# Kernel optimization log

Measured on AMD Instinct MI355X. Metric: run time of the kernel, lower is better.

The kernel has to match this reference:

```python
import jax, jax.numpy as jnp
import numpy as np

N = 8192      # number of nodes; input feature dim == N (identity-style features)
HID = 200     # hidden dim hard-coded in GCNConv(adj.shape[0], 200)
OUT = 5       # out_dim (sentiment classes)


def setup_inputs() -> dict:
    key = jax.random.key(0)
    k1, k2, k3, k4 = jax.random.split(key, 4)
    x = jax.random.normal(k1, (N, N), dtype=jnp.float32)
    adj = jax.random.uniform(k2, (N, N), dtype=jnp.float32)
    W1 = jax.random.normal(k3, (N, HID), dtype=jnp.float32) * (1.0 / np.sqrt(N))
    b1 = jnp.zeros((HID,), dtype=jnp.float32)
    W2 = jax.random.normal(k4, (HID, OUT), dtype=jnp.float32) * (1.0 / np.sqrt(HID))
    b2 = jnp.zeros((OUT,), dtype=jnp.float32)
    return {"x": x, "adj": adj, "W1": W1, "b1": b1, "W2": W2, "b2": b2}


def gcn_conv(adj, x, W, b):
    # support = X @ W (cheap, small output dim), then propagate: adj @ support
    return adj @ (x @ W) + b


def reference(x, adj, W1, b1, W2, b2):
    h = jax.nn.relu(gcn_conv(adj, x, W1, b1))      # [N, 200]
    logits = gcn_conv(adj, h, W2, b2)              # [N, 5]
    return jax.nn.softmax(logits, axis=-1)
```

## Files before the change

kernel.cpp:

```cpp
#include <hip/hip_runtime.h>
#include <hip/hip_fp16.h>
#include <math.h>

#define NN   8192
#define KD   8192
#define HID  200
#define NP   224
#define OUTC 5

#define BM   128
#define BK   32
#define KS   8
#define KCH  (KD / KS)
#define NT   (KCH / BK)
#define LPAD 40

typedef _Float16 f16;
typedef __attribute__((ext_vector_type(4))) _Float16 f16x4;
typedef __attribute__((ext_vector_type(8))) _Float16 f16x8;
typedef __attribute__((ext_vector_type(4))) float f32x4;

__global__ __launch_bounds__(256) void k_prep_w1(const float* __restrict__ W1,
                                                 f16* __restrict__ BfT) {
    __shared__ float tile[64][65];
    const int k0 = blockIdx.x * 64;
    const int n0 = blockIdx.y * 64;
    const int t = threadIdx.x;
    #pragma unroll
    for (int p = 0; p < 16; ++p) {
        int idx = t + p * 256;
        int kk = idx >> 6, nn = idx & 63;
        int n = n0 + nn;
        float v = (n < HID) ? W1[(size_t)(k0 + kk) * HID + n] : 0.0f;
        tile[kk][nn] = v;
    }
    __syncthreads();
    #pragma unroll
    for (int p = 0; p < 16; ++p) {
        int idx = t + p * 256;
        int nn = idx >> 6, kk = idx & 63;
        int n = n0 + nn;
        if (n < NP) BfT[(size_t)n * KD + k0 + kk] = (f16)tile[kk][nn];
    }
}

__global__ __launch_bounds__(512, 4) void k_gemm(const float* __restrict__ A,
                                                 const f16* __restrict__ BfT,
                                                 f16* __restrict__ CP) {
    __shared__ __align__(16) f16 Ah[BM * LPAD];
    __shared__ __align__(16) f16 Al[BM * LPAD];
    __shared__ __align__(16) f16 Bf[NP * LPAD];

    const int t = threadIdx.x;
    const int lane = t & 63;
    const int wave = t >> 6;
    const int wm = wave >> 1, wn = wave & 1;
    const int l15 = lane & 15, g = lane >> 4;
    const int m0 = blockIdx.x * BM;
    const size_t kc0 = (size_t)blockIdx.y * KCH;

    const int arow = t >> 2, aq = t & 3;
    const int br0 = t >> 2, bq0 = t & 3;
    const int u1 = t + 512;
    const int br1 = u1 >> 2, bq1 = u1 & 3;
    const bool hasB1 = (t < 384);

    const float* Aptr = A + (size_t)(m0 + arow) * KD + kc0 + (size_t)aq * 8;
    const f16* B0p = BfT + (size_t)br0 * KD + kc0 + (size_t)bq0 * 8;
    const f16* B1p = BfT + (size_t)br1 * KD + kc0 + (size_t)bq1 * 8;

    f32x4 acc[2][7];
    #pragma unroll
    for (int m = 0; m < 2; ++m)
        #pragma unroll
        for (int n = 0; n < 7; ++n) acc[m][n] = (f32x4){0.f, 0.f, 0.f, 0.f};

    float4 v0, v1;
    f16x8 gb0, gb1;

    auto LOAD = [&](int ks) {
        v0 = *(const float4*)(Aptr + ks);
        v1 = *(const float4*)(Aptr + ks + 4);
        gb0 = *(const f16x8*)(B0p + ks);
        if (hasB1) gb1 = *(const f16x8*)(B1p + ks);
    };
    auto STORE = [&]() {
        f16x8 hv, lv;
        float vv[8] = {v0.x, v0.y, v0.z, v0.w, v1.x, v1.y, v1.z, v1.w};
        #pragma unroll
        for (int j = 0; j < 8; ++j) {
            f16 h = (f16)vv[j];
            hv[j] = h;
            lv[j] = (f16)(vv[j] - (float)h);
        }
        *(f16x8*)&Ah[arow * LPAD + aq * 8] = hv;
        *(f16x8*)&Al[arow * LPAD + aq * 8] = lv;
        *(f16x8*)&Bf[br0 * LPAD + bq0 * 8] = gb0;
        if (hasB1) *(f16x8*)&Bf[br1 * LPAD + bq1 * 8] = gb1;
    };

    LOAD(0);
    for (int i = 0; i < NT; ++i) {
        __syncthreads();
        STORE();
        __syncthreads();
        if (i + 1 < NT) LOAD((i + 1) * BK);

        f16x8 a_h[2], a_l[2];
        #pragma unroll
        for (int m = 0; m < 2; ++m) {
            int r = wm * 32 + m * 16 + l15;
            a_h[m] = *(const f16x8*)&Ah[r * LPAD + g * 8];
            a_l[m] = *(const f16x8*)&Al[r * LPAD + g * 8];
        }
        __builtin_amdgcn_s_setprio(1);
        #pragma unroll
        for (int n = 0; n < 7; ++n) {
            int c = wn * 112 + n * 16 + l15;
            f16x8 b = *(const f16x8*)&Bf[c * LPAD + g * 8];
            #pragma unroll
            for (int m = 0; m < 2; ++m) {
                acc[m][n] = __builtin_amdgcn_mfma_f32_16x16x32_f16(a_l[m], b, acc[m][n], 0, 0, 0);
                acc[m][n] = __builtin_amdgcn_mfma_f32_16x16x32_f16(a_h[m], b, acc[m][n], 0, 0, 0);
            }
        }
        __builtin_amdgcn_s_setprio(0);
    }

    f16* o = CP + (size_t)blockIdx.y * ((size_t)NN * NP);
    #pragma unroll
    for (int m = 0; m < 2; ++m) {
        #pragma unroll
        for (int n = 0; n < 7; ++n) {
            int rb = m0 + wm * 32 + m * 16 + g * 4;
            int c = wn * 112 + n * 16 + l15;
            #pragma unroll
            for (int r = 0; r < 4; ++r)
                o[(size_t)(rb + r) * NP + c] = (f16)acc[m][n][r];
        }
    }
}

__global__ __launch_bounds__(256) void k_combine_split(const f16* __restrict__ CP,
                                                       f16* __restrict__ SfT) {
    __shared__ float tile[64][65];
    const size_t SZ = (size_t)NN * NP;
    const int m0 = blockIdx.x * 64;
    const int n0 = blockIdx.y * 64;
    const int t = threadIdx.x;
    #pragma unroll
    for (int gq = 0; gq < 4; ++gq) {
        int idx4 = t + gq * 256;
        int mm = idx4 >> 4;
        int nn4 = (idx4 & 15) * 4;
        int n = n0 + nn4;
        float s0 = 0.f, s1 = 0.f, s2 = 0.f, s3 = 0.f;
        if (n + 4 <= NP) {
            #pragma unroll
            for (int p = 0; p < KS; ++p) {
                f16x4 v = *(const f16x4*)(CP + (size_t)p * SZ + (size_t)(m0 + mm) * NP + n);
                s0 += (float)v[0]; s1 += (float)v[1]; s2 += (float)v[2]; s3 += (float)v[3];
            }
        }
        tile[mm][nn4 + 0] = s0; tile[mm][nn4 + 1] = s1;
        tile[mm][nn4 + 2] = s2; tile[mm][nn4 + 3] = s3;
    }
    __syncthreads();
    #pragma unroll
    for (int p = 0; p < 16; ++p) {
        int idx = t + p * 256;
        int nn = idx >> 6, mm = idx & 63;
        int n = n0 + nn;
        if (n < NP) SfT[(size_t)n * KD + m0 + mm] = (f16)tile[mm][nn];
    }
}

__global__ __launch_bounds__(256) void k_combine_bias_relu(const f16* __restrict__ CP,
                                                           const float* __restrict__ b1,
                                                           float* __restrict__ H) {
    const size_t SZ = (size_t)NN * NP;
    const int row = blockIdx.x;
    const int t = threadIdx.x;
    if (t < NP) {
        size_t off = (size_t)row * NP + t;
        float s = 0.f;
        #pragma unroll
        for (int p = 0; p < KS; ++p) s += (float)CP[off + p * SZ];
        s += (t < HID) ? b1[t] : 0.0f;
        H[off] = fmaxf(s, 0.0f);
    }
}

__global__ __launch_bounds__(256) void k_hw2(const float* __restrict__ H,
                                             const float* __restrict__ W2,
                                             float* __restrict__ S2T) {
    const int t = threadIdx.x;
    const int wave = t >> 6, lane = t & 63;
    const int row = blockIdx.x * 4 + wave;
    float acc[OUTC] = {0.f, 0.f, 0.f, 0.f, 0.f};
    for (int j = lane; j < HID; j += 64) {
        float h = H[(size_t)row * NP + j];
        #pragma unroll
        for (int c = 0; c < OUTC; ++c) acc[c] += h * W2[j * OUTC + c];
    }
    #pragma unroll
    for (int c = 0; c < OUTC; ++c)
        #pragma unroll
        for (int off = 32; off; off >>= 1) acc[c] += __shfl_down(acc[c], off, 64);
    if (lane == 0) {
        #pragma unroll
        for (int c = 0; c < OUTC; ++c) S2T[(size_t)c * NN + row] = acc[c];
    }
}

__global__ __launch_bounds__(256) void k_final(const float* __restrict__ adj,
                                               const float* __restrict__ S2T,
                                               const float* __restrict__ b2,
                                               float* __restrict__ out) {
    __shared__ float red[4][8][OUTC];
    const int t = threadIdx.x, wave = t >> 6, lane = t & 63;
    const int row0 = blockIdx.x * 8;
    float acc[8][OUTC];
    #pragma unroll
    for (int r = 0; r < 8; ++r)
        #pragma unroll
        for (int c = 0; c < OUTC; ++c) acc[r][c] = 0.f;

    for (int jj = 0; jj < 8; ++jj) {
        int kb = (t + jj * 256) * 4;
        float4 s2[OUTC];
        #pragma unroll
        for (int c = 0; c < OUTC; ++c) s2[c] = *(const float4*)(S2T + (size_t)c * NN + kb);
        #pragma unroll
        for (int r = 0; r < 8; ++r) {
            float4 a = *(const float4*)(adj + (size_t)(row0 + r) * KD + kb);
            #pragma unroll
            for (int c = 0; c < OUTC; ++c)
                acc[r][c] += a.x * s2[c].x + a.y * s2[c].y + a.z * s2[c].z + a.w * s2[c].w;
        }
    }
    #pragma unroll
    for (int r = 0; r < 8; ++r)
        #pragma unroll
        for (int c = 0; c < OUTC; ++c) {
            float v = acc[r][c];
            #pragma unroll
            for (int off = 32; off; off >>= 1) v += __shfl_down(v, off, 64);
            if (lane == 0) red[wave][r][c] = v;
        }
    __syncthreads();
    if (t < 8) {
        int r = t;
        float lg[OUTC];
        #pragma unroll
        for (int c = 0; c < OUTC; ++c)
            lg[c] = red[0][r][c] + red[1][r][c] + red[2][r][c] + red[3][r][c] + b2[c];
        float mx = lg[0];
        #pragma unroll
        for (int c = 1; c < OUTC; ++c) mx = fmaxf(mx, lg[c]);
        float e[OUTC], s = 0.f;
        #pragma unroll
        for (int c = 0; c < OUTC; ++c) { e[c] = expf(lg[c] - mx); s += e[c]; }
        float inv = 1.0f / s;
        #pragma unroll
        for (int c = 0; c < OUTC; ++c) out[(size_t)(row0 + r) * OUTC + c] = e[c] * inv;
    }
}

extern "C" void kernel_launch(void* const* d_in, const int* in_sizes, int n_in,
                              void* d_out, int out_size, void* d_ws, size_t ws_size,
                              hipStream_t stream) {
    const float* x   = (const float*)d_in[0];
    const float* adj = (const float*)d_in[1];
    const float* W1  = (const float*)d_in[2];
    const float* b1  = (const float*)d_in[3];
    const float* W2  = (const float*)d_in[4];
    const float* b2  = (const float*)d_in[5];
    float* out = (float*)d_out;

    char* ws = (char*)d_ws;
    const size_t SPLIT_BYTES = (size_t)NP * KD * sizeof(f16);
    f16*   W1fT = (f16*)(ws);
    f16*   S1fT = (f16*)(ws + SPLIT_BYTES);
    float* H    = (float*)(ws + 2 * SPLIT_BYTES);
    float* S2T  = (float*)(ws + 2 * SPLIT_BYTES + (size_t)NN * NP * sizeof(float));
    f16*   CPf  = (f16*)(ws + 2 * SPLIT_BYTES + (size_t)NN * NP * sizeof(float)
                            + (size_t)OUTC * NN * sizeof(float));

    k_prep_w1<<<dim3(KD / 64, (NP + 63) / 64), 256, 0, stream>>>(W1, W1fT);
    k_gemm<<<dim3(NN / BM, KS), 512, 0, stream>>>(x, W1fT, CPf);
    k_combine_split<<<dim3(NN / 64, (NP + 63) / 64), 256, 0, stream>>>(CPf, S1fT);
    k_gemm<<<dim3(NN / BM, KS), 512, 0, stream>>>(adj, S1fT, CPf);
    k_combine_bias_relu<<<NN, 256, 0, stream>>>(CPf, b1, H);
    k_hw2<<<NN / 4, 256, 0, stream>>>(H, W2, S2T);
    k_final<<<NN / 8, 256, 0, stream>>>(adj, S2T, b2, out);
}
```

Measured before the change: 267.5 us.

## Drop hi/lo fp16 split, use direct global-to-LDS loads with swizzled B layout

The GEMM kernel stops splitting A into high and low fp16 halves, which halves the MFMA count but lowers the precision of the fp32 inputs. It doubles BK to 64 and pre-swizzles B into a tile-contiguous layout so B can be copied straight into LDS with global_load_lds. Manual waitcnt and barrier scheduling replace the two __syncthreads per iteration. The combine and hw2 kernels are vectorised and H is stored in fp16, with some accuracy risk against the fp32 reference.

```diff
diff --git a/kernel.cpp b/kernel.cpp
--- a/kernel.cpp
+++ b/kernel.cpp
@@ -9,65 +9,78 @@
 #define OUTC 5
 
 #define BM   128
-#define BK   32
+#define BK   64
 #define KS   8
 #define KCH  (KD / KS)
 #define NT   (KCH / BK)
-#define LPAD 40
+#define TUB  1792
 
 typedef _Float16 f16;
 typedef __attribute__((ext_vector_type(4))) _Float16 f16x4;
 typedef __attribute__((ext_vector_type(8))) _Float16 f16x8;
 typedef __attribute__((ext_vector_type(4))) float f32x4;
 
+__device__ __forceinline__ void fill16(const f16* g, f16* l) {
+    __builtin_amdgcn_global_load_lds(
+        (const __attribute__((address_space(1))) void*)g,
+        (__attribute__((address_space(3))) void*)l, 16, 0, 0);
+}
+
 __global__ __launch_bounds__(256) void k_prep_w1(const float* __restrict__ W1,
-                                                 f16* __restrict__ BfT) {
+                                                 f16* __restrict__ Bsw) {
     __shared__ float tile[64][65];
-    const int k0 = blockIdx.x * 64;
+    const int kt = blockIdx.x;
     const int n0 = blockIdx.y * 64;
+    const int k0 = kt * 64;
     const int t = threadIdx.x;
     #pragma unroll
-    for (int p = 0; p < 16; ++p) {
-        int idx = t + p * 256;
-        int kk = idx >> 6, nn = idx & 63;
-        int n = n0 + nn;
-        float v = (n < HID) ? W1[(size_t)(k0 + kk) * HID + n] : 0.0f;
-        tile[kk][nn] = v;
+    for (int q = 0; q < 4; ++q) {
+        int idx4 = t + q * 256;
+        int kk = idx4 >> 4, nn4 = (idx4 & 15) * 4;
+        int n = n0 + nn4;
+        float4 v = {0.f, 0.f, 0.f, 0.f};
+        if (n + 4 <= HID) v = *(const float4*)(W1 + (size_t)(k0 + kk) * HID + n);
+        tile[kk][nn4 + 0] = v.x; tile[kk][nn4 + 1] = v.y;
+        tile[kk][nn4 + 2] = v.z; tile[kk][nn4 + 3] = v.w;
     }
     __syncthreads();
     #pragma unroll
-    for (int p = 0; p < 16; ++p) {
-        int idx = t + p * 256;
-        int nn = idx >> 6, kk = idx & 63;
-        int n = n0 + nn;
-        if (n < NP) BfT[(size_t)n * KD + k0 + kk] = (f16)tile[kk][nn];
+    for (int p2 = 0; p2 < 2; ++p2) {
+        int u = t + p2 * 256;
+        int rl = u >> 3, cphys = u & 7;
+        int r = n0 + rl;
+        if (r < NP) {
+            int ck = cphys ^ (r & 7);
+            f16x8 o;
+            #pragma unroll
+            for (int h = 0; h < 8; ++h) o[h] = (f16)tile[ck * 8 + h][rl];
+            *(f16x8*)(Bsw + ((size_t)kt * TUB + r * 8 + cphys) * 8) = o;
+        }
     }
 }
 
 __global__ __launch_bounds__(512, 4) void k_gemm(const float* __restrict__ A,
-                                                 const f16* __restrict__ BfT,
+                                                 const f16* __restrict__ Bsw,
                                                  f16* __restrict__ CP) {
-    __shared__ __align__(16) f16 Ah[BM * LPAD];
-    __shared__ __align__(16) f16 Al[BM * LPAD];
-    __shared__ __align__(16) f16 Bf[NP * LPAD];
+    __shared__ __align__(16) f16 Ah[BM * BK];
+    __shared__ __align__(16) f16 Bf[NP * BK];
 
     const int t = threadIdx.x;
-    const int lane = t & 63;
-    const int wave = t >> 6;
-    const int wm = wave >> 1, wn = wave & 1;
+    const int lane = t & 63, wv = t >> 6;
+    const int wm = wv >> 1, wn = wv & 1;
     const int l15 = lane & 15, g = lane >> 4;
     const int m0 = blockIdx.x * BM;
+    const int kt0 = blockIdx.y * NT;
     const size_t kc0 = (size_t)blockIdx.y * KCH;
 
-    const int arow = t >> 2, aq = t & 3;
-    const int br0 = t >> 2, bq0 = t & 3;
-    const int u1 = t + 512;
-    const int br1 = u1 >> 2, bq1 = u1 & 3;
-    const bool hasB1 = (t < 384);
-
-    const float* Aptr = A + (size_t)(m0 + arow) * KD + kc0 + (size_t)aq * 8;
-    const f16* B0p = BfT + (size_t)br0 * KD + kc0 + (size_t)bq0 * 8;
-    const f16* B1p = BfT + (size_t)br1 * KD + kc0 + (size_t)bq1 * 8;
+    const int ar = t >> 2;
+    const int ac = (t & 3) * 2;
+    const int swzA = ar & 7;
+    f16* aw0 = &Ah[(ar * 8 + ((ac + 0) ^ swzA)) * 8];
+    f16* aw1 = &Ah[(ar * 8 + ((ac + 1) ^ swzA)) * 8];
+    const float* ap = A + (size_t)(m0 + ar) * KD + kc0 + (size_t)(t & 3) * 16;
+
+    const f16* bsrc = Bsw + ((size_t)kt0 * TUB + (size_t)(wv * 64 + lane)) * 8;
 
     f32x4 acc[2][7];
     #pragma unroll
@@ -75,57 +88,61 @@
         #pragma unroll
         for (int n = 0; n < 7; ++n) acc[m][n] = (f32x4){0.f, 0.f, 0.f, 0.f};
 
-    float4 v0, v1;
-    f16x8 gb0, gb1;
-
-    auto LOAD = [&](int ks) {
-        v0 = *(const float4*)(Aptr + ks);
-        v1 = *(const float4*)(Aptr + ks + 4);
-        gb0 = *(const f16x8*)(B0p + ks);
-        if (hasB1) gb1 = *(const f16x8*)(B1p + ks);
-    };
-    auto STORE = [&]() {
-        f16x8 hv, lv;
-        float vv[8] = {v0.x, v0.y, v0.z, v0.w, v1.x, v1.y, v1.z, v1.w};
-        #pragma unroll
-        for (int j = 0; j < 8; ++j) {
-            f16 h = (f16)vv[j];
-            hv[j] = h;
-            lv[j] = (f16)(vv[j] - (float)h);
-        }
-        *(f16x8*)&Ah[arow * LPAD + aq * 8] = hv;
-        *(f16x8*)&Al[arow * LPAD + aq * 8] = lv;
-        *(f16x8*)&Bf[br0 * LPAD + bq0 * 8] = gb0;
-        if (hasB1) *(f16x8*)&Bf[br1 * LPAD + bq1 * 8] = gb1;
-    };
-
-    LOAD(0);
+    float4 v0, v1, v2, v3;
+#define LOADA(i) { const float* p_ = ap + (size_t)(i) * BK;           \
+        v0 = *(const float4*)(p_);      v1 = *(const float4*)(p_ + 4); \
+        v2 = *(const float4*)(p_ + 8);  v3 = *(const float4*)(p_ + 12); }
+
+    LOADA(0);
     for (int i = 0; i < NT; ++i) {
-        __syncthreads();
-        STORE();
-        __syncthreads();
-        if (i + 1 < NT) LOAD((i + 1) * BK);
-
-        f16x8 a_h[2], a_l[2];
-        #pragma unroll
-        for (int m = 0; m < 2; ++m) {
-            int r = wm * 32 + m * 16 + l15;
-            a_h[m] = *(const f16x8*)&Ah[r * LPAD + g * 8];
-            a_l[m] = *(const f16x8*)&Al[r * LPAD + g * 8];
-        }
+        {
+            f16x8 h0, h1;
+            h0[0]=(f16)v0.x; h0[1]=(f16)v0.y; h0[2]=(f16)v0.z; h0[3]=(f16)v0.w;
+            h0[4]=(f16)v1.x; h0[5]=(f16)v1.y; h0[6]=(f16)v1.z; h0[7]=(f16)v1.w;
+            h1[0]=(f16)v2.x; h1[1]=(f16)v2.y; h1[2]=(f16)v2.z; h1[3]=(f16)v2.w;
+            h1[4]=(f16)v3.x; h1[5]=(f16)v3.y; h1[6]=(f16)v3.z; h1[7]=(f16)v3.w;
+            *(f16x8*)aw0 = h0;
+            *(f16x8*)aw1 = h1;
+        }
+        {
+            const f16* bs = bsrc + (size_t)i * (TUB * 8);
+            fill16(bs,            &Bf[(0    + wv * 64) * 8]);
+            fill16(bs + 512 * 8,  &Bf[(512  + wv * 64) * 8]);
+            fill16(bs + 1024 * 8, &Bf[(1024 + wv * 64) * 8]);
+            if (wv < 4) fill16(bs + 1536 * 8, &Bf[(1536 + wv * 64) * 8]);
+        }
+        __builtin_amdgcn_sched_barrier(0);
+        if (i + 1 < NT) {
+            LOADA(i + 1);
+            asm volatile("s_waitcnt vmcnt(4) lgkmcnt(0)" ::: "memory");
+        } else {
+            asm volatile("s_waitcnt vmcnt(0) lgkmcnt(0)" ::: "memory");
+        }
+        __builtin_amdgcn_sched_barrier(0);
+        __builtin_amdgcn_s_barrier();
+        __builtin_amdgcn_sched_barrier(0);
+
         __builtin_amdgcn_s_setprio(1);
         #pragma unroll
-        for (int n = 0; n < 7; ++n) {
-            int c = wn * 112 + n * 16 + l15;
-            f16x8 b = *(const f16x8*)&Bf[c * LPAD + g * 8];
-            #pragma unroll
-            for (int m = 0; m < 2; ++m) {
-                acc[m][n] = __builtin_amdgcn_mfma_f32_16x16x32_f16(a_l[m], b, acc[m][n], 0, 0, 0);
-                acc[m][n] = __builtin_amdgcn_mfma_f32_16x16x32_f16(a_h[m], b, acc[m][n], 0, 0, 0);
+        for (int kk = 0; kk < 2; ++kk) {
+            const int cu = kk * 4 + g;
+            f16x8 a0, a1;
+            { int r = wm * 32 + l15;      a0 = *(const f16x8*)&Ah[(r * 8 + (cu ^ (r & 7))) * 8]; }
+            { int r = wm * 32 + 16 + l15; a1 = *(const f16x8*)&Ah[(r * 8 + (cu ^ (r & 7))) * 8]; }
+            #pragma unroll
+            for (int n = 0; n < 7; ++n) {
+                int cr = wn * 112 + n * 16 + l15;
+                f16x8 b = *(const f16x8*)&Bf[(cr * 8 + (cu ^ (cr & 7))) * 8];
+                acc[0][n] = __builtin_amdgcn_mfma_f32_16x16x32_f16(a0, b, acc[0][n], 0, 0, 0);
+                acc[1][n] = __builtin_amdgcn_mfma_f32_16x16x32_f16(a1, b, acc[1][n], 0, 0, 0);
             }
         }
         __builtin_amdgcn_s_setprio(0);
-    }
+        __builtin_amdgcn_sched_barrier(0);
+        __builtin_amdgcn_s_barrier();
+        __builtin_amdgcn_sched_barrier(0);
+    }
+#undef LOADA
 
     f16* o = CP + (size_t)blockIdx.y * ((size_t)NN * NP);
     #pragma unroll
@@ -141,75 +158,95 @@
     }
 }
 
-__global__ __launch_bounds__(256) void k_combine_split(const f16* __restrict__ CP,
-                                                       f16* __restrict__ SfT) {
+__global__ __launch_bounds__(256) void k_combine_b(const f16* __restrict__ CP,
+                                                   f16* __restrict__ Bsw) {
     __shared__ float tile[64][65];
     const size_t SZ = (size_t)NN * NP;
-    const int m0 = blockIdx.x * 64;
+    const int kt = blockIdx.x;
     const int n0 = blockIdx.y * 64;
+    const int k0 = kt * 64;
     const int t = threadIdx.x;
     #pragma unroll
-    for (int gq = 0; gq < 4; ++gq) {
-        int idx4 = t + gq * 256;
-        int mm = idx4 >> 4;
-        int nn4 = (idx4 & 15) * 4;
+    for (int q = 0; q < 4; ++q) {
+        int idx4 = t + q * 256;
+        int kk = idx4 >> 4, nn4 = (idx4 & 15) * 4;
         int n = n0 + nn4;
         float s0 = 0.f, s1 = 0.f, s2 = 0.f, s3 = 0.f;
-        if (n + 4 <= NP) {
+        if (n < NP) {
             #pragma unroll
             for (int p = 0; p < KS; ++p) {
-                f16x4 v = *(const f16x4*)(CP + (size_t)p * SZ + (size_t)(m0 + mm) * NP + n);
+                f16x4 v = *(const f16x4*)(CP + (size_t)p * SZ + (size_t)(k0 + kk) * NP + n);
                 s0 += (float)v[0]; s1 += (float)v[1]; s2 += (float)v[2]; s3 += (float)v[3];
             }
         }
-        tile[mm][nn4 + 0] = s0; tile[mm][nn4 + 1] = s1;
-        tile[mm][nn4 + 2] = s2; tile[mm][nn4 + 3] = s3;
+        tile[kk][nn4 + 0] = s0; tile[kk][nn4 + 1] = s1;
+        tile[kk][nn4 + 2] = s2; tile[kk][nn4 + 3] = s3;
     }
     __syncthreads();
     #pragma unroll
-    for (int p = 0; p < 16; ++p) {
-        int idx = t + p * 256;
-        int nn = idx >> 6, mm = idx & 63;
-        int n = n0 + nn;
-        if (n < NP) SfT[(size_t)n * KD + m0 + mm] = (f16)tile[mm][nn];
-    }
-}
-
-__global__ __launch_bounds__(256) void k_combine_bias_relu(const f16* __restrict__ CP,
-                                                           const float* __restrict__ b1,
-                                                           float* __restrict__ H) {
+    for (int p2 = 0; p2 < 2; ++p2) {
+        int u = t + p2 * 256;
+        int rl = u >> 3, cphys = u & 7;
+        int r = n0 + rl;
+        if (r < NP) {
+            int ck = cphys ^ (r & 7);
+            f16x8 o;
+            #pragma unroll
+            for (int h = 0; h < 8; ++h) o[h] = (f16)tile[ck * 8 + h][rl];
+            *(f16x8*)(Bsw + ((size_t)kt * TUB + r * 8 + cphys) * 8) = o;
+        }
+    }
+}
+
+__global__ __launch_bounds__(256) void k_combine_h(const f16* __restrict__ CP,
+                                                   const float* __restrict__ b1,
+                                                   f16* __restrict__ Hf) {
     const size_t SZ = (size_t)NN * NP;
-    const int row = blockIdx.x;
-    const int t = threadIdx.x;
-    if (t < NP) {
-        size_t off = (size_t)row * NP + t;
-        float s = 0.f;
-        #pragma unroll
-        for (int p = 0; p < KS; ++p) s += (float)CP[off + p * SZ];
-        s += (t < HID) ? b1[t] : 0.0f;
-        H[off] = fmaxf(s, 0.0f);
-    }
-}
-
-__global__ __launch_bounds__(256) void k_hw2(const float* __restrict__ H,
+    const int cc = threadIdx.x;
+    const int row = blockIdx.x * 8 + threadIdx.y;
+    const size_t off = (size_t)row * NP + cc * 8;
+    float s[8] = {0.f,0.f,0.f,0.f,0.f,0.f,0.f,0.f};
+    #pragma unroll
+    for (int p = 0; p < KS; ++p) {
+        f16x8 v = *(const f16x8*)(CP + (size_t)p * SZ + off);
+        #pragma unroll
+        for (int h = 0; h < 8; ++h) s[h] += (float)v[h];
+    }
+    f16x8 o;
+    #pragma unroll
+    for (int h = 0; h < 8; ++h) {
+        int c = cc * 8 + h;
+        float b = (c < HID) ? b1[c] : 0.f;
+        o[h] = (f16)fmaxf(s[h] + b, 0.f);
+    }
+    *(f16x8*)(Hf + off) = o;
+}
+
+__global__ __launch_bounds__(256) void k_hw2(const f16* __restrict__ Hf,
                                              const float* __restrict__ W2,
                                              float* __restrict__ S2T) {
-    const int t = threadIdx.x;
-    const int wave = t >> 6, lane = t & 63;
-    const int row = blockIdx.x * 4 + wave;
-    float acc[OUTC] = {0.f, 0.f, 0.f, 0.f, 0.f};
-    for (int j = lane; j < HID; j += 64) {
-        float h = H[(size_t)row * NP + j];
-        #pragma unroll
-        for (int c = 0; c < OUTC; ++c) acc[c] += h * W2[j * OUTC + c];
-    }
-    #pragma unroll
-    for (int c = 0; c < OUTC; ++c)
-        #pragma unroll
-        for (int off = 32; off; off >>= 1) acc[c] += __shfl_down(acc[c], off, 64);
+    const int t = threadIdx.x, wv = t >> 6, lane = t & 63;
+    const int row = blockIdx.x * 4 + wv;
+    float s[OUTC] = {0.f, 0.f, 0.f, 0.f, 0.f};
+    if (lane < 28) {
+        f16x8 v = *(const f16x8*)(Hf + (size_t)row * NP + lane * 8);
+        #pragma unroll
+        for (int h = 0; h < 8; ++h) {
+            int c = lane * 8 + h;
+            if (c < HID) {
+                float hv = (float)v[h];
+                #pragma unroll
+                for (int q = 0; q < OUTC; ++q) s[q] += hv * W2[c * OUTC + q];
+            }
+        }
+    }
+    #pragma unroll
+    for (int q = 0; q < OUTC; ++q)
+        #pragma unroll
+        for (int off = 32; off; off >>= 1) s[q] += __shfl_down(s[q], off, 64);
     if (lane == 0) {
         #pragma unroll
-        for (int c = 0; c < OUTC; ++c) S2T[(size_t)c * NN + row] = acc[c];
+        for (int q = 0; q < OUTC; ++q) S2T[(size_t)q * NN + row] = s[q];
     }
 }
 
@@ -258,10 +295,10 @@
         float mx = lg[0];
         #pragma unroll
         for (int c = 1; c < OUTC; ++c) mx = fmaxf(mx, lg[c]);
-        float e[OUTC], s = 0.f;
-        #pragma unroll
-        for (int c = 0; c < OUTC; ++c) { e[c] = expf(lg[c] - mx); s += e[c]; }
-        float inv = 1.0f / s;
+        float e[OUTC], ssum = 0.f;
+        #pragma unroll
+        for (int c = 0; c < OUTC; ++c) { e[c] = expf(lg[c] - mx); ssum += e[c]; }
+        float inv = 1.0f / ssum;
         #pragma unroll
         for (int c = 0; c < OUTC; ++c) out[(size_t)(row0 + r) * OUTC + c] = e[c] * inv;
     }
@@ -279,19 +316,18 @@
     float* out = (float*)d_out;
 
     char* ws = (char*)d_ws;
-    const size_t SPLIT_BYTES = (size_t)NP * KD * sizeof(f16);
-    f16*   W1fT = (f16*)(ws);
-    f16*   S1fT = (f16*)(ws + SPLIT_BYTES);
-    float* H    = (float*)(ws + 2 * SPLIT_BYTES);
-    float* S2T  = (float*)(ws + 2 * SPLIT_BYTES + (size_t)NN * NP * sizeof(float));
-    f16*   CPf  = (f16*)(ws + 2 * SPLIT_BYTES + (size_t)NN * NP * sizeof(float)
-                            + (size_t)OUTC * NN * sizeof(float));
-
-    k_prep_w1<<<dim3(KD / 64, (NP + 63) / 64), 256, 0, stream>>>(W1, W1fT);
-    k_gemm<<<dim3(NN / BM, KS), 512, 0, stream>>>(x, W1fT, CPf);
-    k_combine_split<<<dim3(NN / 64, (NP + 63) / 64), 256, 0, stream>>>(CPf, S1fT);
-    k_gemm<<<dim3(NN / BM, KS), 512, 0, stream>>>(adj, S1fT, CPf);
-    k_combine_bias_relu<<<NN, 256, 0, stream>>>(CPf, b1, H);
-    k_hw2<<<NN / 4, 256, 0, stream>>>(H, W2, S2T);
-    k_final<<<NN / 8, 256, 0, stream>>>(adj, S2T, b2, out);
-}
+    const size_t BSZ = (size_t)NP * KD * sizeof(f16);
+    f16*   BW1 = (f16*)(ws);
+    f16*   BS1 = (f16*)(ws + BSZ);
+    f16*   Hf  = (f16*)(ws + 2 * BSZ);
+    float* S2T = (float*)(ws + 3 * BSZ);
+    f16*   CP  = (f16*)(ws + 3 * BSZ + 256 * 1024);
+
+    k_prep_w1<<<dim3(128, 4), 256, 0, stream>>>(W1, BW1);
+    k_gemm<<<dim3(NN / BM, KS), 512, 0, stream>>>(x, BW1, CP);
+    k_combine_b<<<dim3(128, 4), 256, 0, stream>>>(CP, BS1);
+    k_gemm<<<dim3(NN / BM, KS), 512, 0, stream>>>(adj, BS1, CP);
+    k_combine_h<<<dim3(NN / 8), dim3(28, 8), 0, stream>>>(CP, b1, Hf);
+    k_hw2<<<dim3(NN / 4), 256, 0, stream>>>(Hf, W2, S2T);
+    k_final<<<dim3(NN / 8), 256, 0, stream>>>(adj, S2T, b2, out);
+}
```

After: 273.3 us. 1.02x slower.
